# Optimization experiments

Hardware: AMD Instinct MI355X
Metric: run time of the kernel (lower is better)

Reference implementation:

```python
import jax, jax.numpy as jnp
import numpy as np

B, C, N = 32, 1, 4096
H, W = 64, 64
K, D = 1024, 256  # codebook size, embedding dim


def setup_inputs() -> dict:
    key = jax.random.key(0)
    k0, k1 = jax.random.split(key)
    indices = jax.random.randint(k0, (B, C, N), 0, K, dtype=jnp.int64)
    embedding = jax.random.normal(k1, (K, D), dtype=jnp.float32)
    return {"indices": indices, "embedding": embedding, "h": H, "w": W}


def reference(indices, embedding, h, w):
    b, c, n = indices.shape
    flat = indices.reshape(b * c * n)
    # one-hot @ embedding  ==  direct gather (same math, memory-bound form)
    z_q = jnp.take(embedding, flat, axis=0)        # (b*c*n, D)
    z_q = z_q.reshape(b, h, w, embedding.shape[1])  # view(shape)
    z_q = jnp.transpose(z_q, (0, 3, 1, 2))          # permute(0,3,1,2)
    return z_q
```

## Files before the change

kernel.cpp:

```cpp
#include <hip/hip_runtime.h>


#define VQ_B 32
#define VQ_N 4096
#define VQ_D 256

__global__ __launch_bounds__(256) void vq_gather_kernel(
    const int* __restrict__ indices,
    const float* __restrict__ embedding,
    float* __restrict__ out)
{
    const int bid = blockIdx.x;
    const int b  = bid >> 6;
    const int n0 = (bid & 63) << 6;
    const int l  = threadIdx.x & 63;
    const int w  = threadIdx.x >> 6;

    const int n   = n0 + l;
    const int idx = indices[b * VQ_N + n];
    const float4* __restrict__ row = (const float4*)(embedding + idx * VQ_D);

    const int out_base = b * (VQ_D * VQ_N) + n;

    #pragma unroll
    for (int i = 0; i < 16; ++i) {
        const int c = i * 4 + w;
        const float4 v = row[c];
        const int d = c << 2;
        out[out_base + (d + 0) * VQ_N] = v.x;
        out[out_base + (d + 1) * VQ_N] = v.y;
        out[out_base + (d + 2) * VQ_N] = v.z;
        out[out_base + (d + 3) * VQ_N] = v.w;
    }
}

extern "C" void kernel_launch(void* const* d_in, const int* in_sizes, int n_in,
                              void* d_out, int out_size, void* d_ws, size_t ws_size,
                              hipStream_t stream) {
    const int*   indices   = (const int*)d_in[0];
    const float* embedding = (const float*)d_in[1];
    float* out = (float*)d_out;

    vq_gather_kernel<<<dim3(VQ_B * (VQ_N / 64)), dim3(256), 0, stream>>>(
        indices, embedding, out);
}
```

Before: 142.9 us.

## Stage gathered rows in LDS to emit float4 transposed stores

Gathers 64 embedding rows per block into a padded LDS tile in two halves of D, then reads them back transposed so each thread writes float4 vectors along N instead of scalar stores. The second half's global loads are issued before the first half is written out, overlapping the gather with the transpose. This is meant to widen the output writes, which were scalar 4-byte stores. The cost is extra LDS traffic, several barriers and more registers.

```diff
diff --git a/kernel.cpp b/kernel.cpp
--- a/kernel.cpp
+++ b/kernel.cpp
@@ -4,33 +4,92 @@
 #define VQ_B 32
 #define VQ_N 4096
 #define VQ_D 256
+#define TILE_N 64
+#define HALF_D 128
+#define LDS_STRIDE 129
 
-__global__ __launch_bounds__(256) void vq_gather_kernel(
+__global__ __launch_bounds__(256, 4) void vq_gather_kernel(
     const int* __restrict__ indices,
     const float* __restrict__ embedding,
     float* __restrict__ out)
 {
+    __shared__ int   s_idx[TILE_N];
+    __shared__ float s_tile[TILE_N * LDS_STRIDE];
+
     const int bid = blockIdx.x;
-    const int b  = bid >> 6;
-    const int n0 = (bid & 63) << 6;
-    const int l  = threadIdx.x & 63;
-    const int w  = threadIdx.x >> 6;
+    const int b   = bid >> 6;
+    const int n0  = (bid & 63) << 6;
+    const int t   = threadIdx.x;
 
-    const int n   = n0 + l;
-    const int idx = indices[b * VQ_N + n];
-    const float4* __restrict__ row = (const float4*)(embedding + idx * VQ_D);
+    if (t < TILE_N) s_idx[t] = indices[b * VQ_N + n0 + t];
+    __syncthreads();
 
-    const int out_base = b * (VQ_D * VQ_N) + n;
+    const int g = t >> 3;
+    const int s = t & 7;
+
+    const int nl = t & 15;
+    const int dg = t >> 4;
+
+    float4 v0[8], v1[8];
 
     #pragma unroll
-    for (int i = 0; i < 16; ++i) {
-        const int c = i * 4 + w;
-        const float4 v = row[c];
-        const int d = c << 2;
-        out[out_base + (d + 0) * VQ_N] = v.x;
-        out[out_base + (d + 1) * VQ_N] = v.y;
-        out[out_base + (d + 2) * VQ_N] = v.z;
-        out[out_base + (d + 3) * VQ_N] = v.w;
+    for (int j = 0; j < 8; ++j) {
+        const int L = j * 32 + g;
+        const int r = L >> 2;
+        const int c = (L & 3) * 8 + s;
+        v0[j] = ((const float4*)(embedding + s_idx[r] * VQ_D))[c];
+    }
+    #pragma unroll
+    for (int j = 0; j < 8; ++j) {
+        const int L = j * 32 + g;
+        const int r = L >> 2;
+        const int c = (L & 3) * 8 + s;
+        const float4 v = v0[j];
+        float* p = &s_tile[r * LDS_STRIDE + c * 4];
+        p[0] = v.x; p[1] = v.y; p[2] = v.z; p[3] = v.w;
+    }
+    __syncthreads();
+
+    #pragma unroll
+    for (int j = 0; j < 8; ++j) {
+        const int L = j * 32 + g;
+        const int r = L >> 2;
+        const int c = (L & 3) * 8 + s;
+        v1[j] = ((const float4*)(embedding + s_idx[r] * VQ_D + HALF_D))[c];
+    }
+
+    #pragma unroll
+    for (int jj = 0; jj < 8; ++jj) {
+        const int d = jj * 16 + dg;
+        float4 o;
+        o.x = s_tile[(4 * nl + 0) * LDS_STRIDE + d];
+        o.y = s_tile[(4 * nl + 1) * LDS_STRIDE + d];
+        o.z = s_tile[(4 * nl + 2) * LDS_STRIDE + d];
+        o.w = s_tile[(4 * nl + 3) * LDS_STRIDE + d];
+        *(float4*)(out + (b * VQ_D + d) * VQ_N + n0 + 4 * nl) = o;
+    }
+    __syncthreads();
+
+    #pragma unroll
+    for (int j = 0; j < 8; ++j) {
+        const int L = j * 32 + g;
+        const int r = L >> 2;
+        const int c = (L & 3) * 8 + s;
+        const float4 v = v1[j];
+        float* p = &s_tile[r * LDS_STRIDE + c * 4];
+        p[0] = v.x; p[1] = v.y; p[2] = v.z; p[3] = v.w;
+    }
+    __syncthreads();
+
+    #pragma unroll
+    for (int jj = 0; jj < 8; ++jj) {
+        const int d = jj * 16 + dg;
+        float4 o;
+        o.x = s_tile[(4 * nl + 0) * LDS_STRIDE + d];
+        o.y = s_tile[(4 * nl + 1) * LDS_STRIDE + d];
+        o.z = s_tile[(4 * nl + 2) * LDS_STRIDE + d];
+        o.w = s_tile[(4 * nl + 3) * LDS_STRIDE + d];
+        *(float4*)(out + (b * VQ_D + HALF_D + d) * VQ_N + n0 + 4 * nl) = o;
     }
 }
 
@@ -41,6 +100,6 @@
     const float* embedding = (const float*)d_in[1];
     float* out = (float*)d_out;
 
-    vq_gather_kernel<<<dim3(VQ_B * (VQ_N / 64)), dim3(256), 0, stream>>>(
+    vq_gather_kernel<<<dim3(VQ_B * (VQ_N / TILE_N)), dim3(256), 0, stream>>>(
         indices, embedding, out);
 }
```

Measured after the change: 140.3 us. No clear change (-1.8%).

## Transpose gathered embedding tiles through LDS for float4 coalesced output stores

Applied to the files above, without the earlier changes.

Restructures the gather so each block handles a 32-channel slice of the embedding for 1024 positions. Indices are staged in shared memory. Each wave gathers 32x32 sub-tiles, transposes them through a padded LDS tile, and writes float4 stores along the N dimension. It also prefetches the next sub-tile's rows in registers while the current one is stored, and it reduces the grid to 1024 blocks. The intent is to replace scalar strided stores with wider coalesced stores, at the cost of LDS traffic and fewer, longer-running blocks.

```diff
diff --git a/kernel.cpp b/kernel.cpp
--- a/kernel.cpp
+++ b/kernel.cpp
@@ -4,33 +4,81 @@
 #define VQ_B 32
 #define VQ_N 4096
 #define VQ_D 256
+#define DC 32
+#define NT 1024
+#define NW 256
+#define NSUB 32
+#define TSTRIDE 34
 
-__global__ __launch_bounds__(256) void vq_gather_kernel(
+__global__ __launch_bounds__(256, 4) void vq_gather_kernel(
     const int* __restrict__ indices,
     const float* __restrict__ embedding,
     float* __restrict__ out)
 {
+    __shared__ int   s_idx[NT];
+    __shared__ float s_tile[4][NSUB * TSTRIDE];
+
     const int bid = blockIdx.x;
-    const int b  = bid >> 6;
-    const int n0 = (bid & 63) << 6;
-    const int l  = threadIdx.x & 63;
-    const int w  = threadIdx.x >> 6;
+    const int nt  = bid & 3;
+    const int dc  = (bid >> 2) & 7;
+    const int b   = bid >> 5;
 
-    const int n   = n0 + l;
-    const int idx = indices[b * VQ_N + n];
-    const float4* __restrict__ row = (const float4*)(embedding + idx * VQ_D);
-
-    const int out_base = b * (VQ_D * VQ_N) + n;
+    const int t = threadIdx.x;
+    const int w = t >> 6;
+    const int l = t & 63;
 
     #pragma unroll
-    for (int i = 0; i < 16; ++i) {
-        const int c = i * 4 + w;
-        const float4 v = row[c];
-        const int d = c << 2;
-        out[out_base + (d + 0) * VQ_N] = v.x;
-        out[out_base + (d + 1) * VQ_N] = v.y;
-        out[out_base + (d + 2) * VQ_N] = v.z;
-        out[out_base + (d + 3) * VQ_N] = v.w;
+    for (int k = 0; k < 4; ++k)
+        s_idx[t + 256 * k] = indices[b * VQ_N + nt * NT + t + 256 * k];
+    __syncthreads();
+
+    const int s  = l & 7;
+    const int nn = l >> 3;
+    const int ss = l & 7;
+    const int dd = l >> 3;
+
+    float* tile = s_tile[w];
+    const float* emb_c = embedding + dc * DC;
+    const int wbase = w * NW;
+
+    float* out_w = out + (b * VQ_D + dc * DC) * VQ_N + nt * NT + wbase;
+
+    float4 v[4], vn[4];
+
+    #pragma unroll
+    for (int k = 0; k < 4; ++k) {
+        const int row = s_idx[wbase + nn + 8 * k];
+        v[k] = ((const float4*)(emb_c + row * VQ_D))[s];
+    }
+
+    for (int si = 0; si < 8; ++si) {
+        if (si < 7) {
+            #pragma unroll
+            for (int k = 0; k < 4; ++k) {
+                const int row = s_idx[wbase + (si + 1) * NSUB + nn + 8 * k];
+                vn[k] = ((const float4*)(emb_c + row * VQ_D))[s];
+            }
+        }
+
+        #pragma unroll
+        for (int k = 0; k < 4; ++k) {
+            float* p = &tile[(nn + 8 * k) * TSTRIDE + 4 * s];
+            p[0] = v[k].x; p[1] = v[k].y; p[2] = v[k].z; p[3] = v[k].w;
+        }
+
+        #pragma unroll
+        for (int q = 0; q < 4; ++q) {
+            const int d = dd + 8 * q;
+            float4 o;
+            o.x = tile[(4 * ss + 0) * TSTRIDE + d];
+            o.y = tile[(4 * ss + 1) * TSTRIDE + d];
+            o.z = tile[(4 * ss + 2) * TSTRIDE + d];
+            o.w = tile[(4 * ss + 3) * TSTRIDE + d];
+            *(float4*)(out_w + d * VQ_N + si * NSUB + 4 * ss) = o;
+        }
+
+        #pragma unroll
+        for (int k = 0; k < 4; ++k) v[k] = vn[k];
     }
 }
 
@@ -41,6 +89,6 @@
     const float* embedding = (const float*)d_in[1];
     float* out = (float*)d_out;
 
-    vq_gather_kernel<<<dim3(VQ_B * (VQ_N / 64)), dim3(256), 0, stream>>>(
+    vq_gather_kernel<<<dim3(VQ_B * 8 * 4), dim3(256), 0, stream>>>(
         indices, embedding, out);
 }
```

New measurement: 141.5 us, median of 2. No clear change (-1.0%).
